# Kernel optimization log

Measured on AMD Instinct MI355X. Metric: run time of the kernel, lower is better.

## Reference

```python
import jax, jax.numpy as jnp
import numpy as np

B, T, S, D = 8, 32, 256, 1024


def setup_inputs() -> dict:
    key = jax.random.key(0)
    ks = jax.random.split(key, 10)
    scale = 1.0 / np.sqrt(D)
    return {
        "source1": jax.random.normal(ks[0], (B, T, D), jnp.float32),
        "source2": jax.random.normal(ks[1], (B, T, D), jnp.float32),
        "memory_bank": jax.random.normal(ks[2], (B, S, D), jnp.float32),
        "source_masks1": jnp.ones((B, T), jnp.float32),
        "source_masks2": jnp.ones((B, T), jnp.float32),
        "W_q1": jax.random.normal(ks[3], (D, D), jnp.float32) * scale,
        "b_q1": jnp.zeros((D,), jnp.float32),
        "W_q2": jax.random.normal(ks[4], (D, D), jnp.float32) * scale,
        "b_q2": jnp.zeros((D,), jnp.float32),
        "W_cate": jax.random.normal(ks[5], (2, 2 * D), jnp.float32) * scale,
        "b_cate": jnp.zeros((2,), jnp.float32),
        "W_v": jax.random.normal(ks[6], (D, D), jnp.float32) * scale,
    }


def reference(source1, source2, memory_bank, source_masks1, source_masks2,
              W_q1, b_q1, W_q2, b_q2, W_cate, b_cate, W_v):
    Bq, Tq, Dd = source1.shape
    # accumulate(): running prefix-mean over the segment axis, then mask.
    denom = jnp.arange(1, Tq + 1, dtype=source1.dtype)[None, :, None]
    s1 = (jnp.cumsum(source1, axis=1) / denom) * source_masks1[:, :, None]
    s2 = (jnp.cumsum(source2, axis=1) / denom) * source_masks2[:, :, None]
    # score(): gated attention scoring.
    q1 = s1 @ W_q1.T + b_q1  # [B,T,D]
    q2 = s2 @ W_q2.T + b_q2  # [B,T,D]
    # tanh gate broadcast over all (tgt, src) pairs -> [B,T,S,D]
    g = jnp.tanh(q1[:, :, None, :] + q2[:, :, None, :] + memory_bank[:, None, :, :])
    # sum_j (g @ W_v.T)[..., j] == g @ sum_j W_v[j, :]
    w_colsum = jnp.sum(W_v, axis=0)              # [D]
    sum_gate = g @ w_colsum                       # [B,T,S]
    # linear_cate(concat([h_s, sum_gate*h_s])) split into two halves
    pa = memory_bank @ W_cate[:, :Dd].T           # [B,S,2]
    pb = memory_bank @ W_cate[:, Dd:].T           # [B,S,2]
    out = pa[:, None, :, :] + sum_gate[..., None] * pb[:, None, :, :] + b_cate
    return out  # [B,T,S,2]
```

## Files before the change

### kernel.cpp

```cpp
#include <hip/hip_runtime.h>
#include <hip/hip_bf16.h>

#define Bb 8
#define Tt 32
#define Ss 256
#define Dd 1024
#define SCALE 2.885390081777927f

typedef short short8 __attribute__((ext_vector_type(8)));
typedef float floatx4 __attribute__((ext_vector_type(4)));

__device__ __forceinline__ unsigned short bf16b(float x) {
    __hip_bfloat16 h = __float2bfloat16(x);
    return *(unsigned short*)&h;
}

__device__ __forceinline__ float dot4(float4 a, float4 b) {
    return a.x * b.x + a.y * b.y + a.z * b.z + a.w * b.w;
}

__device__ __forceinline__ float sigm_term(float q, float m, float w, float acc) {
    float e = __builtin_amdgcn_exp2f(q + m);
    return fmaf(w, __builtin_amdgcn_rcpf(e + 1.f), acc);
}

__global__ __launch_bounds__(256) void prep_kernel(
        const float* __restrict__ src1, const float* __restrict__ src2,
        const float* __restrict__ m1, const float* __restrict__ m2,
        const float* __restrict__ W1, const float* __restrict__ W2,
        const float* __restrict__ Wv,
        unsigned short* __restrict__ W1b, unsigned short* __restrict__ W2b,
        unsigned short* __restrict__ s1b, unsigned short* __restrict__ s2b,
        float* __restrict__ part) {
    const int blk = blockIdx.x, tid = threadIdx.x;
    if (blk < 1024) {
        const int idx = blk * 256 + tid;
        float4 a = ((const float4*)W1)[idx];
        float4 b = ((const float4*)W2)[idx];
        ushort4 oa = { bf16b(a.x), bf16b(a.y), bf16b(a.z), bf16b(a.w) };
        ushort4 ob = { bf16b(b.x), bf16b(b.y), bf16b(b.z), bf16b(b.w) };
        ((ushort4*)W1b)[idx] = oa;
        ((ushort4*)W2b)[idx] = ob;
    } else if (blk < 1088) {
        const int bb = blk - 1024;
        const int db = bb & 3, jc = bb >> 2;
        const int d = db * 256 + tid;
        float a = 0.f;
        const int j0 = jc * 64;
        for (int j = 0; j < 64; j++)
            a += Wv[(size_t)(j0 + j) * Dd + d];
        part[jc * Dd + d] = a;
    } else {
        const int idx = (blk - 1088) * 256 + tid;
        const int srcsel = idx >> 13;
        const int bd = idx & 8191;
        const int b = bd >> 10, d = bd & 1023;
        const float* sp = srcsel ? src2 : src1;
        const float* mp = srcsel ? m2 : m1;
        unsigned short* op = srcsel ? s2b : s1b;
        float a = 0.f;
        for (int t = 0; t < Tt; t++) {
            a += sp[(size_t)(b * Tt + t) * Dd + d];
            float inv = __builtin_amdgcn_rcpf((float)(t + 1));
            op[(size_t)(b * Tt + t) * Dd + d] = bf16b(a * inv * mp[b * Tt + t]);
        }
    }
}

__global__ __launch_bounds__(64) void gemm_kernel(
        const unsigned short* __restrict__ s1b, const unsigned short* __restrict__ s2b,
        const unsigned short* __restrict__ W1b, const unsigned short* __restrict__ W2b,
        const float* __restrict__ bq1, const float* __restrict__ bq2,
        const float* __restrict__ part,
        float* __restrict__ qp, float* __restrict__ wsum) {
    const int blk = blockIdx.x;
    const int lane = threadIdx.x;
    if (blk >= 512) {
        const int d = (blk - 512) * 64 + lane;
        float a = 0.f;
        #pragma unroll
        for (int jc = 0; jc < 16; jc++)
            a += part[jc * Dd + d];
        wsum[d] = a;
        return;
    }
    const int m0 = (blk & 15) * 16;
    const int n0 = (blk >> 4) * 32;
    const int lm = lane & 15;
    const int quad = lane >> 4;

    floatx4 acc0 = {0.f, 0.f, 0.f, 0.f};
    floatx4 acc1 = {0.f, 0.f, 0.f, 0.f};
    const unsigned short* a1p = s1b + (size_t)(m0 + lm) * Dd;
    const unsigned short* a2p = s2b + (size_t)(m0 + lm) * Dd;
    const unsigned short* b1a = W1b + (size_t)(n0 + lm) * Dd;
    const unsigned short* b1b = W1b + (size_t)(n0 + 16 + lm) * Dd;
    const unsigned short* b2a = W2b + (size_t)(n0 + lm) * Dd;
    const unsigned short* b2b = W2b + (size_t)(n0 + 16 + lm) * Dd;

    #pragma unroll 2
    for (int k0 = 0; k0 < Dd; k0 += 32) {
        const int off = k0 + quad * 8;
        short8 a1 = *(const short8*)(a1p + off);
        short8 a2 = *(const short8*)(a2p + off);
        short8 vb1a = *(const short8*)(b1a + off);
        short8 vb2a = *(const short8*)(b2a + off);
        short8 vb1b = *(const short8*)(b1b + off);
        short8 vb2b = *(const short8*)(b2b + off);
        acc0 = __builtin_amdgcn_mfma_f32_16x16x32_bf16(a1, vb1a, acc0, 0, 0, 0);
        acc1 = __builtin_amdgcn_mfma_f32_16x16x32_bf16(a1, vb1b, acc1, 0, 0, 0);
        acc0 = __builtin_amdgcn_mfma_f32_16x16x32_bf16(a2, vb2a, acc0, 0, 0, 0);
        acc1 = __builtin_amdgcn_mfma_f32_16x16x32_bf16(a2, vb2b, acc1, 0, 0, 0);
    }

    const int na = n0 + lm, nb = n0 + 16 + lm;
    const float biasa = bq1[na] + bq2[na];
    const float biasb = bq1[nb] + bq2[nb];
    #pragma unroll
    for (int r = 0; r < 4; r++) {
        const int m = m0 + quad * 4 + r;
        qp[(size_t)m * Dd + na] = SCALE * (acc0[r] + biasa);
        qp[(size_t)m * Dd + nb] = SCALE * (acc1[r] + biasb);
    }
}

__global__ __launch_bounds__(256) void out_kernel(
        const float* __restrict__ qp, const float* __restrict__ mem,
        const float* __restrict__ wsum, const float* __restrict__ Wc,
        const float* __restrict__ bc, float* __restrict__ out) {
    const int wave = threadIdx.x >> 6;
    const int lane = threadIdx.x & 63;
    const int gid = blockIdx.x * 4 + wave;
    const int half = gid >> 11;
    const int bs = gid & 2047;
    const int b = bs >> 8, s = bs & 255;
    const float* mrow = mem + (size_t)bs * Dd;

    float4 mv[4], wv[4];
    float pa0 = 0.f, pa1 = 0.f, pb0 = 0.f, pb1 = 0.f, Wl = 0.f;
    #pragma unroll
    for (int j = 0; j < 4; j++) {
        const int d0 = j * 256 + lane * 4;
        float4 m_ = *(const float4*)(mrow + d0);
        wv[j] = *(const float4*)(wsum + d0);
        Wl += wv[j].x + wv[j].y + wv[j].z + wv[j].w;
        float4 wa0 = *(const float4*)(Wc + d0);
        float4 wa1 = *(const float4*)(Wc + 2048 + d0);
        float4 wb0 = *(const float4*)(Wc + 1024 + d0);
        float4 wb1 = *(const float4*)(Wc + 3072 + d0);
        pa0 += dot4(m_, wa0);
        pa1 += dot4(m_, wa1);
        pb0 += dot4(m_, wb0);
        pb1 += dot4(m_, wb1);
        mv[j].x = m_.x * SCALE; mv[j].y = m_.y * SCALE;
        mv[j].z = m_.z * SCALE; mv[j].w = m_.w * SCALE;
    }
    #pragma unroll
    for (int o = 32; o > 0; o >>= 1) {
        pa0 += __shfl_xor(pa0, o);
        pa1 += __shfl_xor(pa1, o);
        pb0 += __shfl_xor(pb0, o);
        pb1 += __shfl_xor(pb1, o);
        Wl  += __shfl_xor(Wl, o);
    }
    const float C0 = pa0 + Wl * pb0 + bc[0];
    const float C1 = pa1 + Wl * pb1 + bc[1];
    const float D0 = 2.f * pb0, D1 = 2.f * pb1;

    const int t0 = half * 16;
    for (int tp = 0; tp < 16; tp += 2) {
        const float* q0 = qp + (size_t)(b * Tt + t0 + tp) * Dd;
        const float* q1 = q0 + Dd;
        float p0 = 0.f, p1 = 0.f;
        #pragma unroll
        for (int j = 0; j < 4; j++) {
            const int d0 = j * 256 + lane * 4;
            float4 x0 = *(const float4*)(q0 + d0);
            float4 x1 = *(const float4*)(q1 + d0);
            p0 = sigm_term(x0.x, mv[j].x, wv[j].x, p0);
            p0 = sigm_term(x0.y, mv[j].y, wv[j].y, p0);
            p0 = sigm_term(x0.z, mv[j].z, wv[j].z, p0);
            p0 = sigm_term(x0.w, mv[j].w, wv[j].w, p0);
            p1 = sigm_term(x1.x, mv[j].x, wv[j].x, p1);
            p1 = sigm_term(x1.y, mv[j].y, wv[j].y, p1);
            p1 = sigm_term(x1.z, mv[j].z, wv[j].z, p1);
            p1 = sigm_term(x1.w, mv[j].w, wv[j].w, p1);
        }
        #pragma unroll
        for (int o = 32; o > 0; o >>= 1) {
            p0 += __shfl_xor(p0, o);
            p1 += __shfl_xor(p1, o);
        }
        if (lane == 0) {
            const int tA = t0 + tp;
            float2 oA = { C0 - D0 * p0, C1 - D1 * p0 };
            float2 oB = { C0 - D0 * p1, C1 - D1 * p1 };
            *(float2*)(out + ((size_t)(b * Tt + tA) * Ss + s) * 2) = oA;
            *(float2*)(out + ((size_t)(b * Tt + tA + 1) * Ss + s) * 2) = oB;
        }
    }
}

extern "C" void kernel_launch(void* const* d_in, const int* in_sizes, int n_in,
                              void* d_out, int out_size, void* d_ws, size_t ws_size,
                              hipStream_t stream) {
    const float* src1 = (const float*)d_in[0];
    const float* src2 = (const float*)d_in[1];
    const float* mem  = (const float*)d_in[2];
    const float* m1   = (const float*)d_in[3];
    const float* m2   = (const float*)d_in[4];
    const float* Wq1  = (const float*)d_in[5];
    const float* bq1  = (const float*)d_in[6];
    const float* Wq2  = (const float*)d_in[7];
    const float* bq2  = (const float*)d_in[8];
    const float* Wc   = (const float*)d_in[9];
    const float* bc   = (const float*)d_in[10];
    const float* Wv   = (const float*)d_in[11];
    float* out = (float*)d_out;

    char* ws = (char*)d_ws;
    unsigned short* s1b = (unsigned short*)(ws);
    unsigned short* s2b = (unsigned short*)(ws + (512u << 10));
    unsigned short* W1b = (unsigned short*)(ws + (1u << 20));
    unsigned short* W2b = (unsigned short*)(ws + (3u << 20));
    float* qp   = (float*)(ws + (5u << 20));
    float* wsum = (float*)(ws + (6u << 20));
    float* part = (float*)(ws + (6u << 20) + 4096);

    prep_kernel<<<1152, 256, 0, stream>>>(src1, src2, m1, m2, Wq1, Wq2, Wv,
                                          W1b, W2b, s1b, s2b, part);
    gemm_kernel<<<528, 64, 0, stream>>>(s1b, s2b, W1b, W2b, bq1, bq2, part, qp, wsum);
    out_kernel<<<1024, 256, 0, stream>>>(qp, mem, wsum, Wc, bc, out);
}
```

Measured before the change: 128.7 us.

## Register-tile out_kernel over 4x4 (t,s) pairs and precompute memory projections in gemm

The out kernel now gives each wave a 4 target x 4 source tile instead of 16 targets for a single source row. Each loaded q and memory vector is reused four times from registers, which cuts load traffic per sigmoid term. The memory-bank projections against W_cate (pa/pb) move into 2048 extra wave-blocks of the gemm launch, so out_kernel reads a precomputed float4 per (b,s). The trade-offs are higher register pressure from 16 accumulators and 32 float4 temporaries, and an extra read of the memory bank in the gemm stage.

```diff
diff --git a/kernel.cpp b/kernel.cpp
--- a/kernel.cpp
+++ b/kernel.cpp
@@ -71,10 +71,39 @@
         const unsigned short* __restrict__ s1b, const unsigned short* __restrict__ s2b,
         const unsigned short* __restrict__ W1b, const unsigned short* __restrict__ W2b,
         const float* __restrict__ bq1, const float* __restrict__ bq2,
-        const float* __restrict__ part,
-        float* __restrict__ qp, float* __restrict__ wsum) {
+        const float* __restrict__ part, const float* __restrict__ mem,
+        const float* __restrict__ Wc,
+        float* __restrict__ qp, float* __restrict__ wsum,
+        float* __restrict__ pab) {
     const int blk = blockIdx.x;
     const int lane = threadIdx.x;
+    if (blk >= 528) {
+        const int bs = blk - 528;
+        const float4* mrow = (const float4*)mem + (size_t)bs * 256;
+        const float4* Wc4 = (const float4*)Wc;
+        float a0 = 0.f, a1 = 0.f, b0 = 0.f, b1 = 0.f;
+        #pragma unroll
+        for (int j = 0; j < 4; j++) {
+            const int idx = j * 64 + lane;
+            float4 m_ = mrow[idx];
+            a0 += dot4(m_, Wc4[idx]);
+            b0 += dot4(m_, Wc4[256 + idx]);
+            a1 += dot4(m_, Wc4[512 + idx]);
+            b1 += dot4(m_, Wc4[768 + idx]);
+        }
+        #pragma unroll
+        for (int o = 32; o > 0; o >>= 1) {
+            a0 += __shfl_xor(a0, o);
+            a1 += __shfl_xor(a1, o);
+            b0 += __shfl_xor(b0, o);
+            b1 += __shfl_xor(b1, o);
+        }
+        if (lane == 0) {
+            float4 r = { a0, a1, b0, b1 };
+            ((float4*)pab)[bs] = r;
+        }
+        return;
+    }
     if (blk >= 512) {
         const int d = (blk - 512) * 64 + lane;
         float a = 0.f;
@@ -126,77 +155,96 @@
 
 __global__ __launch_bounds__(256) void out_kernel(
         const float* __restrict__ qp, const float* __restrict__ mem,
-        const float* __restrict__ wsum, const float* __restrict__ Wc,
+        const float* __restrict__ wsum, const float* __restrict__ pab,
         const float* __restrict__ bc, float* __restrict__ out) {
     const int wave = threadIdx.x >> 6;
     const int lane = threadIdx.x & 63;
     const int gid = blockIdx.x * 4 + wave;
-    const int half = gid >> 11;
-    const int bs = gid & 2047;
-    const int b = bs >> 8, s = bs & 255;
-    const float* mrow = mem + (size_t)bs * Dd;
-
-    float4 mv[4], wv[4];
-    float pa0 = 0.f, pa1 = 0.f, pb0 = 0.f, pb1 = 0.f, Wl = 0.f;
+    const int b = gid >> 9;
+    const int r = gid & 511;
+    const int tq = r >> 6, sq = r & 63;
+    const int t0 = tq * 4, s0 = sq * 4;
+    const int bs0 = b * Ss + s0;
+
+    const float4* mem4 = (const float4*)mem;
+    const float4* q4 = (const float4*)qp;
+    const float4* wsum4 = (const float4*)wsum;
+
+    float4 wv[4];
+    float Wl = 0.f;
     #pragma unroll
     for (int j = 0; j < 4; j++) {
-        const int d0 = j * 256 + lane * 4;
-        float4 m_ = *(const float4*)(mrow + d0);
-        wv[j] = *(const float4*)(wsum + d0);
+        wv[j] = wsum4[j * 64 + lane];
         Wl += wv[j].x + wv[j].y + wv[j].z + wv[j].w;
-        float4 wa0 = *(const float4*)(Wc + d0);
-        float4 wa1 = *(const float4*)(Wc + 2048 + d0);
-        float4 wb0 = *(const float4*)(Wc + 1024 + d0);
-        float4 wb1 = *(const float4*)(Wc + 3072 + d0);
-        pa0 += dot4(m_, wa0);
-        pa1 += dot4(m_, wa1);
-        pb0 += dot4(m_, wb0);
-        pb1 += dot4(m_, wb1);
-        mv[j].x = m_.x * SCALE; mv[j].y = m_.y * SCALE;
-        mv[j].z = m_.z * SCALE; mv[j].w = m_.w * SCALE;
-    }
-    #pragma unroll
-    for (int o = 32; o > 0; o >>= 1) {
-        pa0 += __shfl_xor(pa0, o);
-        pa1 += __shfl_xor(pa1, o);
-        pb0 += __shfl_xor(pb0, o);
-        pb1 += __shfl_xor(pb1, o);
-        Wl  += __shfl_xor(Wl, o);
-    }
-    const float C0 = pa0 + Wl * pb0 + bc[0];
-    const float C1 = pa1 + Wl * pb1 + bc[1];
-    const float D0 = 2.f * pb0, D1 = 2.f * pb1;
-
-    const int t0 = half * 16;
-    for (int tp = 0; tp < 16; tp += 2) {
-        const float* q0 = qp + (size_t)(b * Tt + t0 + tp) * Dd;
-        const float* q1 = q0 + Dd;
-        float p0 = 0.f, p1 = 0.f;
-        #pragma unroll
-        for (int j = 0; j < 4; j++) {
-            const int d0 = j * 256 + lane * 4;
-            float4 x0 = *(const float4*)(q0 + d0);
-            float4 x1 = *(const float4*)(q1 + d0);
-            p0 = sigm_term(x0.x, mv[j].x, wv[j].x, p0);
-            p0 = sigm_term(x0.y, mv[j].y, wv[j].y, p0);
-            p0 = sigm_term(x0.z, mv[j].z, wv[j].z, p0);
-            p0 = sigm_term(x0.w, mv[j].w, wv[j].w, p0);
-            p1 = sigm_term(x1.x, mv[j].x, wv[j].x, p1);
-            p1 = sigm_term(x1.y, mv[j].y, wv[j].y, p1);
-            p1 = sigm_term(x1.z, mv[j].z, wv[j].z, p1);
-            p1 = sigm_term(x1.w, mv[j].w, wv[j].w, p1);
-        }
-        #pragma unroll
-        for (int o = 32; o > 0; o >>= 1) {
-            p0 += __shfl_xor(p0, o);
-            p1 += __shfl_xor(p1, o);
-        }
-        if (lane == 0) {
-            const int tA = t0 + tp;
-            float2 oA = { C0 - D0 * p0, C1 - D1 * p0 };
-            float2 oB = { C0 - D0 * p1, C1 - D1 * p1 };
-            *(float2*)(out + ((size_t)(b * Tt + tA) * Ss + s) * 2) = oA;
-            *(float2*)(out + ((size_t)(b * Tt + tA + 1) * Ss + s) * 2) = oB;
+    }
+    #pragma unroll
+    for (int o = 32; o > 0; o >>= 1) Wl += __shfl_xor(Wl, o);
+
+    const float bc0 = bc[0], bc1 = bc[1];
+    float C0[4], C1[4], D0[4], D1[4];
+    #pragma unroll
+    for (int si = 0; si < 4; si++) {
+        float4 pv = ((const float4*)pab)[bs0 + si];
+        C0[si] = pv.x + Wl * pv.z + bc0;
+        C1[si] = pv.y + Wl * pv.w + bc1;
+        D0[si] = 2.f * pv.z;
+        D1[si] = 2.f * pv.w;
+    }
+
+    float p[4][4];
+    #pragma unroll
+    for (int ti = 0; ti < 4; ti++)
+        #pragma unroll
+        for (int si = 0; si < 4; si++) p[ti][si] = 0.f;
+
+    #pragma unroll
+    for (int j = 0; j < 4; j++) {
+        const int idx = j * 64 + lane;
+        float4 mj[4], qj[4];
+        #pragma unroll
+        for (int si = 0; si < 4; si++) {
+            float4 m_ = mem4[(size_t)(bs0 + si) * 256 + idx];
+            mj[si].x = m_.x * SCALE; mj[si].y = m_.y * SCALE;
+            mj[si].z = m_.z * SCALE; mj[si].w = m_.w * SCALE;
+        }
+        #pragma unroll
+        for (int ti = 0; ti < 4; ti++)
+            qj[ti] = q4[(size_t)(b * Tt + t0 + ti) * 256 + idx];
+        const float4 w_ = wv[j];
+        #pragma unroll
+        for (int ti = 0; ti < 4; ti++) {
+            #pragma unroll
+            for (int si = 0; si < 4; si++) {
+                float acc = p[ti][si];
+                acc = sigm_term(qj[ti].x, mj[si].x, w_.x, acc);
+                acc = sigm_term(qj[ti].y, mj[si].y, w_.y, acc);
+                acc = sigm_term(qj[ti].z, mj[si].z, w_.z, acc);
+                acc = sigm_term(qj[ti].w, mj[si].w, w_.w, acc);
+                p[ti][si] = acc;
+            }
+        }
+    }
+
+    #pragma unroll
+    for (int ti = 0; ti < 4; ti++)
+        #pragma unroll
+        for (int si = 0; si < 4; si++) {
+            float v = p[ti][si];
+            #pragma unroll
+            for (int o = 32; o > 0; o >>= 1) v += __shfl_xor(v, o);
+            p[ti][si] = v;
+        }
+
+    if (lane == 0) {
+        #pragma unroll
+        for (int ti = 0; ti < 4; ti++) {
+            const size_t rowo = ((size_t)(b * Tt + t0 + ti) * Ss + s0) * 2;
+            #pragma unroll
+            for (int si = 0; si < 4; si++) {
+                float2 o2 = { C0[si] - D0[si] * p[ti][si],
+                              C1[si] - D1[si] * p[ti][si] };
+                *(float2*)(out + rowo + si * 2) = o2;
+            }
         }
     }
 }
@@ -226,9 +274,11 @@
     float* qp   = (float*)(ws + (5u << 20));
     float* wsum = (float*)(ws + (6u << 20));
     float* part = (float*)(ws + (6u << 20) + 4096);
+    float* pab  = (float*)(ws + (6u << 20) + 4096 + 65536);
 
     prep_kernel<<<1152, 256, 0, stream>>>(src1, src2, m1, m2, Wq1, Wq2, Wv,
                                           W1b, W2b, s1b, s2b, part);
-    gemm_kernel<<<528, 64, 0, stream>>>(s1b, s2b, W1b, W2b, bq1, bq2, part, qp, wsum);
-    out_kernel<<<1024, 256, 0, stream>>>(qp, mem, wsum, Wc, bc, out);
-}
+    gemm_kernel<<<2576, 64, 0, stream>>>(s1b, s2b, W1b, W2b, bq1, bq2, part,
+                                         mem, Wc, qp, wsum, pab);
+    out_kernel<<<1024, 256, 0, stream>>>(qp, mem, wsum, pab, bc, out);
+}
```

New measurement: 126.0 us. -2.1%, faster.
